# Kernel tuning notes

Hardware: AMD Instinct MI355X
Metric: run time of the kernel (lower is better)

The kernel has to match this reference:

```python
import jax, jax.numpy as jnp
import numpy as np

B, P, N, H, W = 8, 4096, 1024, 1024, 1024


def setup_inputs() -> dict:
    key = jax.random.key(0)
    k1, k2, k3, k4 = jax.random.split(key, 4)
    return {
        "pred_points": jax.random.uniform(k1, (B, P, 2), dtype=jnp.float32),
        "dicts_coords": jax.random.uniform(k2, (B, N, 2), dtype=jnp.float32),
        "dicts_keys": jax.random.randint(k3, (B, N), 0, 1024, dtype=jnp.int64) if jax.config.jax_enable_x64 else jax.random.randint(k3, (B, N), 0, 1024).astype(jnp.int32),
        "masks": jax.random.randint(k4, (B, H, W), 0, 1025).astype(jnp.int32),
    }


def _match_single(U, V, keys, lm):
    # U: [P,2] normalized points, V: [N,2] gt coords, keys: [N] ids, lm: [H,W] label map
    h, w = lm.shape
    x = jnp.clip(jnp.round(U[:, 0] * h).astype(jnp.int32), 0, h - 1)
    y = jnp.clip(jnp.round(U[:, 1] * w).astype(jnp.int32), 0, w - 1)
    labels = lm[x, y]                                   # [P] label at each point
    # inside[j, p] == (mask for gt j covers point p); mask j is label channel keys[j]+1
    inside = labels[None, :] == (keys + 1)[:, None]     # [N,P] bool
    # full euclidean distance matrix gt->points
    D = jnp.sqrt(jnp.sum((V[:, None, :] - U[None, :, :]) ** 2, axis=-1))  # [N,P]
    inside_any = inside.any(axis=0)                     # points inside ANY mask
    avail0 = inside_any
    bg0 = ~inside_any                                   # background points
    idx = jnp.arange(U.shape[0])
    BIG = jnp.asarray(1e30, D.dtype)

    def step(carry, xs):
        avail, bg = carry
        ins_j, d_j = xs
        cand = ins_j & avail
        cnt = cand.sum()
        d_in = jnp.where(cand, d_j, BIG)
        u_in = jnp.argmin(d_in)                         # first-index tiebreak, like list order
        d_bg = jnp.where(bg, d_j, BIG)
        u_bg = jnp.argmin(d_bg)
        has_bg = bg.any()
        use_in = cnt > 0
        u = jnp.where(use_in, u_in, jnp.where(has_bg, u_bg, -1))
        cost = jnp.where(use_in, d_in[u_in], jnp.where(has_bg, d_bg[u_bg], jnp.asarray(0.0, D.dtype)))
        # inside-match consumes u from available; multi-point case dumps others into bg
        avail = jnp.where(use_in, avail & (idx != u_in), avail)
        others = cand & (idx != u_in)
        bg = jnp.where(use_in,
                       jnp.where(cnt > 1, bg | others, bg),
                       jnp.where(has_bg, bg & (idx != u_bg), bg))
        return (avail, bg), (u, cost)

    _, (src, costs) = jax.lax.scan(step, (avail0, bg0), (inside, D))
    tgt = jnp.where(src >= 0, jnp.arange(V.shape[0]), -1)
    return src, tgt, costs.sum()


def reference(pred_points, dicts_coords, dicts_keys, masks):
    # Returns padded matches per batch: src[b,j] = matched point index for gt j (-1 if skipped),
    # tgt[b,j] = j when matched else -1, total_cost[b] = sum of matched distances.
    src, tgt, total_cost = jax.vmap(_match_single)(pred_points, dicts_coords, dicts_keys, masks)
    return src, tgt, total_cost
```

## Files before the change

kernel.cpp:

```cpp
#include <hip/hip_runtime.h>
#include <stdint.h>

#define PPTS 4096
#define NGT  1024
#define HH   1024
#define WW   1024
#define EVPOOL_CAP 3072
#define BGCAP 160
#define RB 12

#define PART_BYTES (8 * 8 * 1025 * 2)
#define LAB_OFF    PART_BYTES
#define SPILL_OFF  (LAB_OFF + 8 * PPTS * 2)
#define SPILL_CAP  2048
#define WS_NEED    (SPILL_OFF + 8 * SPILL_CAP * 2)

typedef unsigned long long u64;

__device__ __forceinline__ float pdist2(float vx, float vy, float ux, float uy) {
    float dx = __fsub_rn(vx, ux);
    float dy = __fsub_rn(vy, uy);
    return __fadd_rn(__fmul_rn(dx, dx), __fmul_rn(dy, dy));
}

__global__ __launch_bounds__(512) void label_kernel(
    const float* __restrict__ pred, const int* __restrict__ masks,
    unsigned short* __restrict__ part, unsigned short* __restrict__ labs)
{
    __shared__ int lh[1025];
    const int blk = blockIdx.x, b = blk >> 3, sb = blk & 7;
    const int t = threadIdx.x;
    lh[t] = 0; lh[t + 512] = 0;
    if (t == 0) lh[1024] = 0;
    __syncthreads();
    const int p = (sb << 9) + t;
    float2 u = ((const float2*)(pred + (size_t)b * PPTS * 2))[p];
    int xi = (int)rintf(__fmul_rn(u.x, 1024.0f));
    int yi = (int)rintf(__fmul_rn(u.y, 1024.0f));
    xi = min(max(xi, 0), HH - 1);
    yi = min(max(yi, 0), WW - 1);
    int lab = (masks + (size_t)b * HH * WW)[xi * WW + yi];
    labs[(size_t)b * PPTS + p] = (unsigned short)lab;
    atomicAdd(&lh[lab], 1);
    __syncthreads();
    unsigned short* Pp = part + (size_t)b * 8200 + sb * 1025;
    Pp[t] = (unsigned short)lh[t];
    Pp[t + 512] = (unsigned short)lh[t + 512];
    if (t == 0) Pp[1024] = (unsigned short)lh[1024];
}

__global__ __launch_bounds__(1024) void matcher_kernel(
    const float* __restrict__ pred,
    const float* __restrict__ coords,
    const int*   __restrict__ keys,
    const int*   __restrict__ masks,
    float* __restrict__ out,
    const unsigned short* __restrict__ part, const unsigned short* __restrict__ labs,
    unsigned short* __restrict__ spill, int useWs, int B)
{
    __shared__ __align__(16) char regU[32768];
    __shared__ __align__(8)  char regE[8192];
    __shared__ __align__(8)  char regB[8200];
    __shared__ __align__(8)  char regP[2 * EVPOOL_CAP];
    __shared__ __align__(4)  char regS[384];
    __shared__ __align__(8)  char regT[2048];
    __shared__ u64            wScr64[16];
    __shared__ u64            sTot;
    __shared__ unsigned short evAx[1024];
    __shared__ unsigned short occList[NGT];
    __shared__ short          matchU[NGT];
    __shared__ unsigned       bgbits[PPTS / 32];
    __shared__ int            scal[4];
    __shared__ float2         vLds[NGT];

    float2*         bucketC  = (float2*)regU;
    unsigned short* ldsEnt   = (unsigned short*)regE;
    int*            bEnd     = (int*)regB;
    int*            occA     = ((int*)regB) + 1025;
    u64*            specWin  = (u64*)regB;
    int*            firstOcc = (int*)regP;
    unsigned short* evPool   = (unsigned short*)regP;
    unsigned*       present  = (unsigned*)regS;
    unsigned short* bgListSh = (unsigned short*)regS;
    unsigned short* bSt      = (unsigned short*)regT;
    float2*         vSteps   = (float2*)regT;
    int*   wScrI = (int*)wScr64;
    float* wScrF = (float*)wScr64;

    const int b = blockIdx.x;
    const int t = threadIdx.x;
    const int lane = t & 63, wv = t >> 6;
    const float* Ub = pred   + (size_t)b * PPTS * 2;
    const float2* Ub2 = (const float2*)Ub;
    const float* Vb = coords + (size_t)b * NGT * 2;
    const float2* Vb2 = (const float2*)Vb;
    const int*   Kb = keys   + (size_t)b * NGT;
    unsigned short* evSpillB = spill + (size_t)b * SPILL_CAP;
    const int spillCap = useWs ? SPILL_CAP : 0;

    if (t < PPTS / 32) bgbits[t] = 0;
    if (t == 0) scal[0] = 0;
    const int k1 = Kb[t] + 1;
    const float2 vMe = Vb2[t];
    vLds[t] = vMe;
    int lab[4]; float2 up[4];
    #pragma unroll
    for (int i = 0; i < 4; i++) up[i] = Ub2[t + (i << 10)];
    occA[t] = 0; firstOcc[t] = 0x7FFFFFFF;
    if (t == 0) { occA[1024] = 0; firstOcc[1024] = 0x7FFFFFFF; }
    if (t < 33) present[t] = 0;
    if (useWs) {
        const unsigned short* Pb = part + (size_t)b * 8200;
        int s = 0;
        #pragma unroll
        for (int sb = 0; sb < 8; sb++) s += Pb[sb * 1025 + t];
        bEnd[t] = s;
        if (t == 0) {
            int s2 = 0;
            #pragma unroll
            for (int sb = 0; sb < 8; sb++) s2 += Pb[sb * 1025 + 1024];
            bEnd[1024] = s2;
        }
        const unsigned short* Lb = labs + (size_t)b * PPTS;
        #pragma unroll
        for (int i = 0; i < 4; i++) lab[i] = Lb[t + (i << 10)];
    } else {
        bEnd[t] = 0;
        if (t == 0) bEnd[1024] = 0;
    }
    __syncthreads();
    atomicOr(&present[k1 >> 5], 1u << (k1 & 31));
    atomicAdd(&occA[k1], 1);
    atomicMin(&firstOcc[k1], t);
    if (!useWs) {
        const int* Mb = masks + (size_t)b * HH * WW;
        #pragma unroll
        for (int i = 0; i < 4; i++) {
            float2 u = up[i];
            int xi = (int)rintf(__fmul_rn(u.x, 1024.0f));
            int yi = (int)rintf(__fmul_rn(u.y, 1024.0f));
            xi = min(max(xi, 0), HH - 1);
            yi = min(max(yi, 0), WW - 1);
            lab[i] = Mb[xi * WW + yi];
            atomicAdd(&bEnd[lab[i]], 1);
        }
    }
    __syncthreads();

    {
        int c0 = bEnd[t], o0 = occA[t];
        bool pr0 = (present[t >> 5] >> (t & 31)) & 1u;
        int bCnt = bEnd[k1];
        int fo   = firstOcc[k1];
        int evc  = (fo == t && bCnt > 0) ? (bCnt - 1) : 0;
        u64 myv = (pr0 ? ((u64)(unsigned)c0 << 32) : ((u64)(unsigned)c0 << 48))
                  | ((u64)(unsigned)evc << 16) | (u64)(unsigned)o0;
        u64 add1 = 0; bool pr1 = false;
        if (t == 1023) {
            int c1 = bEnd[1024], o1 = occA[1024];
            pr1 = present[32] & 1u;
            add1 = (pr1 ? ((u64)(unsigned)c1 << 32) : ((u64)(unsigned)c1 << 48))
                   | (u64)(unsigned)o1;
        }
        u64 tot = myv + add1;
        u64 inc = tot;
        #pragma unroll
        for (int off = 1; off < 64; off <<= 1) {
            u64 n = __shfl_up(inc, off, 64);
            if (lane >= off) inc += n;
        }
        if (lane == 63) wScr64[wv] = inc;
        __syncthreads();
        if (t < 16) {
            u64 v = wScr64[t], inc2 = v;
            #pragma unroll
            for (int off = 1; off < 16; off <<= 1) {
                u64 n = __shfl_up(inc2, off, 64);
                if (t >= off) inc2 += n;
            }
            wScr64[t] = inc2 - v;
            if (t == 15) sTot = inc2;
        }
        __syncthreads();
        u64 excl = wScr64[wv] + inc - tot;
        int nBg0v = (int)(sTot >> 48);
        int bgS = (int)(excl >> 48);
        int prS = (int)((excl >> 32) & 0xFFFF);
        int evS = (int)((excl >> 16) & 0xFFFF);
        int ocS = (int)(excl & 0xFFFF);
        int start0 = pr0 ? (nBg0v + prS) : bgS;
        bEnd[t] = start0;
        occA[t] = ocS;
        evAx[t] = (unsigned short)evS;
        if (t >= 1) bSt[t - 1] = (unsigned short)start0;
        if (t == 1023) {
            u64 ex1 = excl + myv;
            int bgS1 = (int)(ex1 >> 48);
            int prS1 = (int)((ex1 >> 32) & 0xFFFF);
            int start1 = pr1 ? (nBg0v + prS1) : bgS1;
            bEnd[1024] = start1; occA[1024] = (int)(ex1 & 0xFFFF);
            bSt[1023] = (unsigned short)start1;
        }
    }
    __syncthreads();
    const int nBg0  = (int)(sTot >> 48);
    const int totEv = (int)((sTot >> 16) & 0xFFFF);
    const int EVcap = min(EVPOOL_CAP, PPTS - nBg0);

    #pragma unroll
    for (int i = 0; i < 4; i++) {
        int p = t + (i << 10);
        int slot = atomicAdd(&bEnd[lab[i]], 1);
        ldsEnt[slot] = (unsigned short)p;
        bucketC[slot] = up[i];
    }
    {
        int slot = atomicAdd(&occA[k1], 1);
        occList[slot] = (unsigned short)t;
    }
    __syncthreads();

    float costPartial = 0.0f;
    {
        const int l = t + 1;
        const int os = occA[t], oe = occA[l];
        for (int i = os + 1; i < oe; i++) {
            unsigned short v = occList[i];
            int k = i - 1;
            while (k >= os && occList[k] > v) { occList[k + 1] = occList[k]; k--; }
            occList[k + 1] = v;
        }
        const int bs = bSt[t], be = bEnd[l];
        const int bn = be - bs;
        if (oe > os && bn > 0 && bn <= RB) {
            float rcx[RB], rcy[RB]; int rp[RB];
            #pragma unroll
            for (int k = 0; k < RB; k++)
                if (k < bn) { float2 c = bucketC[bs + k]; rcx[k] = c.x; rcy[k] = c.y;
                              rp[k] = ldsEnt[bs + k]; }
            unsigned cons = 0;
            for (int o = os; o < oe; o++) {
                int j = occList[o];
                float2 v = vLds[j];
                u64 best = ~0ull;
                #pragma unroll
                for (int k = 0; k < RB; k++) {
                    if (k < bn && !((cons >> k) & 1u)) {
                        float d2 = pdist2(v.x, v.y, rcx[k], rcy[k]);
                        u64 pk = ((u64)__float_as_uint(d2) << 24)
                                 | ((u64)(unsigned)rp[k] << 12) | (u64)(unsigned)k;
                        if (pk < best) best = pk;
                    }
                }
                if (best != ~0ull) {
                    int eW = (int)(best & 0xFFFull);
                    matchU[j] = (short)((best >> 12) & 0xFFFull);
                    costPartial = __fadd_rn(costPartial,
                        __fsqrt_rn(__uint_as_float((unsigned)(best >> 24))));
                    cons |= 1u << eW;
                    if (o == os) {
                        int base = evAx[j];
                        #pragma unroll
                        for (int k = 0; k < RB; k++) {
                            if (k < bn && k != eW) {
                                int idx = base + k - (k > eW ? 1 : 0);
                                if (idx < EVcap) evPool[idx] = (unsigned short)(bs + k);
                                else if (idx - EVcap < spillCap)
                                    evSpillB[idx - EVcap] = (unsigned short)rp[k];
                            }
                        }
                    }
                } else matchU[j] = -2;
            }
        } else if (oe > os) {
            u64 cons = 0;
            for (int o = os; o < oe; o++) {
                int j = occList[o];
                float2 v = vLds[j];
                u64 best = ~0ull;
                int avail = 0;
                for (int e = bs; e < be; e++) {
                    int eIdx = e - bs;
                    int p = ldsEnt[e];
                    bool consd;
                    if (eIdx < 64) consd = (cons >> eIdx) & 1ull;
                    else {
                        consd = false;
                        for (int o2 = os; o2 < o; o2++)
                            if ((int)matchU[occList[o2]] == p) { consd = true; break; }
                    }
                    if (consd) continue;
                    avail++;
                    float2 u = bucketC[e];
                    float d2 = pdist2(v.x, v.y, u.x, u.y);
                    u64 pk = ((u64)__float_as_uint(d2) << 24) | ((u64)(unsigned)p << 12)
                             | (u64)(unsigned)eIdx;
                    if (pk < best) best = pk;
                }
                if (avail > 0) {
                    int eW = (int)(best & 0xFFFull);
                    matchU[j] = (short)((best >> 12) & 0xFFFull);
                    costPartial = __fadd_rn(costPartial,
                        __fsqrt_rn(__uint_as_float((unsigned)(best >> 24))));
                    if (eW < 64) cons |= 1ull << eW;
                    if (o == os) {
                        int base = evAx[j], w3 = 0;
                        for (int e = bs; e < be; e++) {
                            if (e - bs == eW) continue;
                            int idx = base + w3;
                            if (idx < EVcap) evPool[idx] = (unsigned short)e;
                            else if (idx - EVcap < spillCap)
                                evSpillB[idx - EVcap] = ldsEnt[e];
                            w3++;
                        }
                    }
                } else matchU[j] = -2;
            }
        }
    }
    __syncthreads();

    {
        bool need = (matchU[t] == (short)-2);
        u64 m = __ballot(need);
        if (lane == 0) wScrI[wv] = __popcll(m);
    }
    __syncthreads();
    if (t < 64) {
        int orig = (t < 16) ? wScrI[t] : 0;
        int v = orig;
        #pragma unroll
        for (int off = 1; off <= 8; off <<= 1) {
            int n = __shfl_up(v, off, 64);
            if (t >= off) v += n;
        }
        if (t < 16) wScrI[t] = v - orig;
        if (t == 15) scal[0] = v;
    }
    __syncthreads();
    {
        bool need = (matchU[t] == (short)-2);
        u64 m = __ballot(need);
        if (need) {
            int rank = __popcll(m & ((1ull << lane) - 1ull));
            int idx = wScrI[wv] + rank;
            if (idx < BGCAP) { bgListSh[idx] = (unsigned short)t; vSteps[idx] = vMe; }
        }
    }
    __syncthreads();

    const int bgCnt = min(scal[0], BGCAP);
    {
        const int nStage = min(totEv, EVcap);
        float2 sc[4]; unsigned short sp[4];
        #pragma unroll
        for (int k = 0; k < 4; k++) {
            int i = t + (k << 10);
            if (i < nStage) { int slot = evPool[i]; sp[k] = ldsEnt[slot]; sc[k] = bucketC[slot]; }
        }
        __syncthreads();
        #pragma unroll
        for (int k = 0; k < 4; k++) {
            int i = t + (k << 10);
            if (i < nStage) { ldsEnt[nBg0 + i] = sp[k]; bucketC[nBg0 + i] = sc[k]; }
        }
    }
    __syncthreads();

    for (int base5 = wv * 5; base5 < bgCnt; base5 += 80) {
        u64 best[5]; float vxq[5], vyq[5]; int limq[5];
        int maxLim = 0;
        #pragma unroll
        for (int q = 0; q < 5; q++) {
            int s = base5 + q;
            best[q] = ~0ull; limq[q] = 0; vxq[q] = 0.0f; vyq[q] = 0.0f;
            if (s < bgCnt) {
                int js = bgListSh[s];
                float2 v = vSteps[s];
                vxq[q] = v.x; vyq[q] = v.y;
                limq[q] = nBg0 + min((int)evAx[js], EVcap);
                maxLim = max(maxLim, limq[q]);
            }
        }
        for (int i = lane; i < maxLim; i += 64) {
            float2 c = bucketC[i];
            unsigned p = ldsEnt[i];
            #pragma unroll
            for (int q = 0; q < 5; q++) {
                if (i < limq[q]) {
                    float d2 = pdist2(vxq[q], vyq[q], c.x, c.y);
                    u64 pk = ((u64)__float_as_uint(d2) << 32) | p;
                    if (pk < best[q]) best[q] = pk;
                }
            }
        }
        #pragma unroll
        for (int q = 0; q < 5; q++) {
            int s = base5 + q;
            if (s < bgCnt) {
                int js = bgListSh[s];
                int ne = evAx[js];
                u64 bq = best[q];
                for (int ei = EVcap + lane; ei < ne; ei += 64) {
                    if (ei - EVcap >= spillCap) break;
                    unsigned p = evSpillB[ei - EVcap];
                    float2 c = Ub2[p];
                    float d2 = pdist2(vxq[q], vyq[q], c.x, c.y);
                    u64 pk = ((u64)__float_as_uint(d2) << 32) | p;
                    if (pk < bq) bq = pk;
                }
                #pragma unroll
                for (int off = 32; off >= 1; off >>= 1) {
                    u64 o = __shfl_xor(bq, off, 64);
                    if (o < bq) bq = o;
                }
                if (lane == 0) specWin[s] = bq;
            }
        }
    }
    __syncthreads();

    {
        int done = 0;
        for (;;) {
            if (t == 0) scal[3] = bgCnt;
            __syncthreads();
            if (t >= done && t < bgCnt) {
                u64 w = specWin[t];
                if (w != ~0ull) {
                    unsigned p = (unsigned)(w & 0xFFFFFFFFull);
                    bool inval = (bgbits[p >> 5] >> (p & 31)) & 1u;
                    if (!inval) {
                        for (int s2 = done; s2 < t; s2++) {
                            u64 w2 = specWin[s2];
                            if (w2 != ~0ull &&
                                (unsigned)(w2 & 0xFFFFFFFFull) == p) { inval = true; break; }
                        }
                    }
                    if (inval) atomicMin(&scal[3], t);
                }
            }
            __syncthreads();
            const int fs = scal[3];
            if (fs >= bgCnt) break;
            if (t >= done && t < fs) {
                u64 w = specWin[t];
                if (w != ~0ull) {
                    unsigned p = (unsigned)(w & 0xFFFFFFFFull);
                    atomicOr(&bgbits[p >> 5], 1u << (p & 31));
                }
            }
            __syncthreads();
            {
                const int js = bgListSh[fs];
                const float2 v = vSteps[fs];
                const int ne = evAx[js];
                const int lim = nBg0 + min(ne, EVcap);
                u64 best = ~0ull;
                for (int i = t; i < lim; i += 1024) {
                    unsigned p = ldsEnt[i];
                    if (!((bgbits[p >> 5] >> (p & 31)) & 1u)) {
                        float2 c = bucketC[i];
                        float d2 = pdist2(v.x, v.y, c.x, c.y);
                        u64 pk = ((u64)__float_as_uint(d2) << 32) | p;
                        if (pk < best) best = pk;
                    }
                }
                for (int ei = EVcap + t; ei < ne; ei += 1024) {
                    if (ei - EVcap >= spillCap) break;
                    unsigned p = evSpillB[ei - EVcap];
                    if (!((bgbits[p >> 5] >> (p & 31)) & 1u)) {
                        float2 c = Ub2[p];
                        float d2 = pdist2(v.x, v.y, c.x, c.y);
                        u64 pk = ((u64)__float_as_uint(d2) << 32) | p;
                        if (pk < best) best = pk;
                    }
                }
                #pragma unroll
                for (int off = 32; off >= 1; off >>= 1) {
                    u64 o = __shfl_xor(best, off, 64);
                    if (o < best) best = o;
                }
                if (lane == 0) wScr64[wv] = best;
                __syncthreads();
                if (t == 0) {
                    u64 bb = wScr64[0];
                    for (int i = 1; i < 16; i++) if (wScr64[i] < bb) bb = wScr64[i];
                    specWin[fs] = bb;
                    if (bb != ~0ull) {
                        unsigned p = (unsigned)(bb & 0xFFFFFFFFull);
                        bgbits[p >> 5] |= 1u << (p & 31);
                    }
                }
            }
            done = fs + 1;
        }
    }
    if (t < bgCnt) {
        const int js = bgListSh[t];
        u64 w0 = specWin[t];
        if (w0 == ~0ull) matchU[js] = -1;
        else {
            matchU[js] = (short)(w0 & 0xFFFFFFFFull);
            costPartial = __fadd_rn(costPartial,
                __fsqrt_rn(__uint_as_float((unsigned)(w0 >> 32))));
        }
    }
    __syncthreads();

    {
        float cp = costPartial;
        #pragma unroll
        for (int off = 32; off >= 1; off >>= 1) cp += __shfl_xor(cp, off, 64);
        if (lane == 0) wScrF[wv] = cp;
    }
    __syncthreads();
    if (t == 0) {
        float tot = 0.0f;
        for (int i = 0; i < 16; ++i) tot = __fadd_rn(tot, wScrF[i]);
        out[(size_t)2 * B * NGT + b] = tot;
    }
    {
        int u = matchU[t];
        out[(size_t)b * NGT + t] = (float)u;
        out[(size_t)B * NGT + (size_t)b * NGT + t] = (u >= 0) ? (float)t : -1.0f;
    }
}

extern "C" void kernel_launch(void* const* d_in, const int* in_sizes, int n_in,
                              void* d_out, int out_size, void* d_ws, size_t ws_size,
                              hipStream_t stream) {
    const float* pred   = (const float*)d_in[0];
    const float* coords = (const float*)d_in[1];
    const int*   keys   = (const int*)d_in[2];
    const int*   masks  = (const int*)d_in[3];
    float* out = (float*)d_out;
    int B = in_sizes[2] / NGT;
    int useWs = (B == 8 && ws_size >= (size_t)WS_NEED) ? 1 : 0;
    unsigned short* partP  = (unsigned short*)d_ws;
    unsigned short* labsP  = (unsigned short*)((char*)d_ws + LAB_OFF);
    unsigned short* spillP = (unsigned short*)((char*)d_ws + SPILL_OFF);
    if (useWs) {
        label_kernel<<<B * 8, 512, 0, stream>>>(pred, masks, partP, labsP);
    }
    matcher_kernel<<<B, 1024, 0, stream>>>(pred, coords, keys, masks, out,
                                           partP, labsP, spillP, useWs, B);
}
```

Before: 119.5 us.

## Replace brute-force background nearest search with uniform-grid ring search

Builds a 32x32 spatial grid over the staged candidate points in shared memory, using an atomic count, a prefix scan and a scatter. Each wave then searches expanding rings of cells around one background ground-truth point, stopping early once the best distance beats the ring gap. The goal is to avoid scanning every candidate for every background gt. In exchange it adds grid-build passes, extra barriers, about 48 KB more shared memory, and poor lane utilisation on the small inner rings, where each ring also pays a wave-wide reduction.

Result: faster. 114.3 us (-4.3%).

```diff
diff --git a/kernel.cpp b/kernel.cpp
--- a/kernel.cpp
+++ b/kernel.cpp
@@ -72,12 +72,16 @@
     __shared__ unsigned       bgbits[PPTS / 32];
     __shared__ int            scal[4];
     __shared__ float2         vLds[NGT];
+    __shared__ unsigned short gIdx[PPTS];
+    __shared__ unsigned short gP[PPTS];
+    __shared__ __align__(16) float2 gC[PPTS];
 
     float2*         bucketC  = (float2*)regU;
     unsigned short* ldsEnt   = (unsigned short*)regE;
     int*            bEnd     = (int*)regB;
     int*            occA     = ((int*)regB) + 1025;
     u64*            specWin  = (u64*)regB;
+    unsigned*       cellCnt  = (unsigned*)(regB + 1280);
     int*            firstOcc = (int*)regP;
     unsigned short* evPool   = (unsigned short*)regP;
     unsigned*       present  = (unsigned*)regS;
@@ -367,55 +371,120 @@
     }
     __syncthreads();
 
-    for (int base5 = wv * 5; base5 < bgCnt; base5 += 80) {
-        u64 best[5]; float vxq[5], vyq[5]; int limq[5];
-        int maxLim = 0;
-        #pragma unroll
-        for (int q = 0; q < 5; q++) {
-            int s = base5 + q;
-            best[q] = ~0ull; limq[q] = 0; vxq[q] = 0.0f; vyq[q] = 0.0f;
-            if (s < bgCnt) {
-                int js = bgListSh[s];
-                float2 v = vSteps[s];
-                vxq[q] = v.x; vyq[q] = v.y;
-                limq[q] = nBg0 + min((int)evAx[js], EVcap);
-                maxLim = max(maxLim, limq[q]);
-            }
-        }
-        for (int i = lane; i < maxLim; i += 64) {
-            float2 c = bucketC[i];
-            unsigned p = ldsEnt[i];
+    if (bgCnt > 0) {
+        const int nT = nBg0 + min(totEv, EVcap);
+        cellCnt[t] = 0;
+        __syncthreads();
+        int myCell[4];
+        #pragma unroll
+        for (int k = 0; k < 4; k++) {
+            int i = t + (k << 10);
+            myCell[k] = -1;
+            if (i < nT) {
+                float2 c = bucketC[i];
+                int cx = min(31, max(0, (int)__fmul_rn(c.x, 32.0f)));
+                int cy = min(31, max(0, (int)__fmul_rn(c.y, 32.0f)));
+                myCell[k] = (cx << 5) | cy;
+                atomicAdd(&cellCnt[myCell[k]], 1);
+            }
+        }
+        __syncthreads();
+        {
+            unsigned c0 = cellCnt[t];
+            unsigned inc = c0;
             #pragma unroll
-            for (int q = 0; q < 5; q++) {
-                if (i < limq[q]) {
-                    float d2 = pdist2(vxq[q], vyq[q], c.x, c.y);
-                    u64 pk = ((u64)__float_as_uint(d2) << 32) | p;
-                    if (pk < best[q]) best[q] = pk;
-                }
-            }
-        }
-        #pragma unroll
-        for (int q = 0; q < 5; q++) {
-            int s = base5 + q;
-            if (s < bgCnt) {
-                int js = bgListSh[s];
-                int ne = evAx[js];
-                u64 bq = best[q];
+            for (int off = 1; off < 64; off <<= 1) {
+                unsigned n = __shfl_up(inc, off, 64);
+                if (lane >= off) inc += n;
+            }
+            if (lane == 63) wScrI[wv] = (int)inc;
+            __syncthreads();
+            if (t < 16) {
+                int v = wScrI[t], inc2 = v;
+                #pragma unroll
+                for (int off = 1; off < 16; off <<= 1) {
+                    int n = __shfl_up(inc2, off, 64);
+                    if (t >= off) inc2 += n;
+                }
+                wScrI[t] = inc2 - v;
+            }
+            __syncthreads();
+            unsigned excl = (unsigned)wScrI[wv] + inc - c0;
+            cellCnt[t] = excl;
+            __syncthreads();
+        }
+        #pragma unroll
+        for (int k = 0; k < 4; k++) {
+            if (myCell[k] >= 0) {
+                int i = t + (k << 10);
+                int slot = atomicAdd(&cellCnt[myCell[k]], 1);
+                gIdx[slot] = (unsigned short)i;
+                gP[slot]   = ldsEnt[i];
+                gC[slot]   = bucketC[i];
+            }
+        }
+        __syncthreads();
+        for (int s = wv; s < bgCnt; s += 16) {
+            const int js = bgListSh[s];
+            const float2 v = vSteps[s];
+            const int lim = nBg0 + min((int)evAx[js], EVcap);
+            const int cx = min(31, max(0, (int)__fmul_rn(v.x, 32.0f)));
+            const int cy = min(31, max(0, (int)__fmul_rn(v.y, 32.0f)));
+            u64 best = ~0ull;
+            for (int r = 0; r <= 31; r++) {
+                if (r >= 1) {
+                    float gap = __fmul_rn((float)(r - 1), 0.03125f) - 1e-6f;
+                    if (gap > 0.0f) {
+                        float bd2 = __uint_as_float((unsigned)(best >> 32));
+                        if (bd2 < __fmul_rn(gap, gap)) break;
+                    }
+                }
+                const int ncells = (r == 0) ? 1 : 8 * r;
+                for (int ci = lane; ci < ncells; ci += 64) {
+                    int dx, dy;
+                    if (r == 0) { dx = 0; dy = 0; }
+                    else if (ci < 2 * r)      { dx = -r + ci;            dy = -r; }
+                    else if (ci < 4 * r)      { dx = r;                  dy = -r + (ci - 2 * r); }
+                    else if (ci < 6 * r)      { dx = r - (ci - 4 * r);   dy = r; }
+                    else                      { dx = -r;                 dy = r - (ci - 6 * r); }
+                    int x = cx + dx, y = cy + dy;
+                    if ((unsigned)x < 32u && (unsigned)y < 32u) {
+                        int c = (x << 5) | y;
+                        int beg = c ? (int)cellCnt[c - 1] : 0;
+                        int end = (int)cellCnt[c];
+                        for (int i2 = beg; i2 < end; i2++) {
+                            if (gIdx[i2] < lim) {
+                                float2 cc = gC[i2];
+                                float d2 = pdist2(v.x, v.y, cc.x, cc.y);
+                                u64 pk = ((u64)__float_as_uint(d2) << 32) | gP[i2];
+                                if (pk < best) best = pk;
+                            }
+                        }
+                    }
+                }
+                #pragma unroll
+                for (int off = 32; off >= 1; off >>= 1) {
+                    u64 o = __shfl_xor(best, off, 64);
+                    if (o < best) best = o;
+                }
+            }
+            const int ne = evAx[js];
+            if (ne > EVcap && spillCap > 0) {
                 for (int ei = EVcap + lane; ei < ne; ei += 64) {
                     if (ei - EVcap >= spillCap) break;
                     unsigned p = evSpillB[ei - EVcap];
                     float2 c = Ub2[p];
-                    float d2 = pdist2(vxq[q], vyq[q], c.x, c.y);
+                    float d2 = pdist2(v.x, v.y, c.x, c.y);
                     u64 pk = ((u64)__float_as_uint(d2) << 32) | p;
-                    if (pk < bq) bq = pk;
+                    if (pk < best) best = pk;
                 }
                 #pragma unroll
                 for (int off = 32; off >= 1; off >>= 1) {
-                    u64 o = __shfl_xor(bq, off, 64);
-                    if (o < bq) bq = o;
-                }
-                if (lane == 0) specWin[s] = bq;
-            }
+                    u64 o = __shfl_xor(best, off, 64);
+                    if (o < best) best = o;
+                }
+            }
+            if (lane == 0) specWin[s] = best;
         }
     }
     __syncthreads();
```
